# Kernel optimization log

Measured on AMD Instinct MI355X. Metric: run time of the kernel, lower is better.

Reference implementation:

```python
import jax, jax.numpy as jnp
import numpy as np

B, N, F, D, H, L, K = 128, 128, 13, 256, 8, 8, 10
FF = 2 * D  # FFN / hidden width
HEAD = D // H


def setup_inputs() -> dict:
    key = jax.random.key(0)
    ks = iter(jax.random.split(key, 64))
    def nrm(shape, scale=0.02):
        return jax.random.normal(next(ks), shape, dtype=jnp.float32) * scale
    return {
        "input_features": jax.random.normal(next(ks), (B, N, F), dtype=jnp.float32),
        "input_points": jax.random.normal(next(ks), (B, N, 2), dtype=jnp.float32),
        "input_mask": jnp.ones((B, N, 1), dtype=jnp.float32),
        "input_time": jax.random.uniform(next(ks), (B, 1), dtype=jnp.float32),
        # get_encoding: Dense(2D, gelu) -> Dense(D, gelu)
        "enc_w1": nrm((F, FF)), "enc_b1": jnp.zeros((FF,), jnp.float32),
        "enc_w2": nrm((FF, D)), "enc_b2": jnp.zeros((D,), jnp.float32),
        # FourierProjection MLP (no bias, swish)
        "four_w1": nrm((D, FF)), "four_w2": nrm((FF, D)),
        # FiLM time projection (no bias)
        "time_w": nrm((D, FF)),
        # local KNN MLPs: round 0 input 2*F, round 1 input 2*D
        "loc1_w1": nrm((2 * F, FF)), "loc1_b1": jnp.zeros((FF,), jnp.float32),
        "loc1_w2": nrm((FF, D)), "loc1_b2": jnp.zeros((D,), jnp.float32),
        "loc2_w1": nrm((2 * D, FF)), "loc2_b1": jnp.zeros((FF,), jnp.float32),
        "loc2_w2": nrm((FF, D)), "loc2_b2": jnp.zeros((D,), jnp.float32),
        # transformer encoder layers, stacked over L
        "qkv_w": nrm((L, D, 3 * D)), "qkv_b": jnp.zeros((L, 3 * D), jnp.float32),
        "out_w": nrm((L, D, D)), "out_b": jnp.zeros((L, D), jnp.float32),
        "ln1_g": jnp.ones((L, D), jnp.float32), "ln1_b": jnp.zeros((L, D), jnp.float32),
        "ff1_w": nrm((L, D, FF)), "ff1_b": jnp.zeros((L, FF), jnp.float32),
        "ff2_w": nrm((L, FF, D)), "ff2_b": jnp.zeros((L, D), jnp.float32),
        "gamma": jnp.full((L, D), 1e-5, dtype=jnp.float32),
        "ln2_g": jnp.ones((L, D), jnp.float32), "ln2_b": jnp.zeros((L, D), jnp.float32),
    }


def _ln(x, g, b, eps=1e-5):
    m = jnp.mean(x, axis=-1, keepdims=True)
    v = jnp.var(x, axis=-1, keepdims=True)
    return (x - m) * jax.lax.rsqrt(v + eps) * g + b


def _fourier(t, w1, w2):
    # t: (B,1) -> (B,D)
    half = D // 2
    emb = np.log(10000.0) / (half - 1)
    freq = jnp.exp(-emb * jnp.arange(half, dtype=jnp.float32))
    angle = t * freq[None, :] * 1000.0  # (B, half)
    e = jnp.concatenate([jnp.sin(angle), jnp.cos(angle)], axis=-1)
    e = jax.nn.silu(e @ w1)
    return jax.nn.silu(e @ w2)


def _get_neighbors(points, feats, w1, b1, w2, b2):
    # points: (B,N,P), feats: (B,N,C) -> (B,N,D)
    r = jnp.sum(points * points, axis=-1)  # (B,N)
    d = r[:, :, None] - 2.0 * jnp.einsum('bnp,bmp->bnm', points, points) + r[:, None, :]
    _, idx = jax.lax.top_k(-d, K + 1)
    idx = idx[:, :, 1:]  # drop self, (B,N,K)
    knn = jax.vmap(lambda f, i: f[i])(feats, idx)  # (B,N,K,C)
    center = jnp.broadcast_to(feats[:, :, None, :], knn.shape)
    local = jnp.concatenate([knn - center, center], axis=-1)  # (B,N,K,2C)
    local = jax.nn.gelu(local @ w1 + b1)
    local = jax.nn.gelu(local @ w2 + b2)
    return jnp.mean(local, axis=2)


def _mha(x, mask, wqkv, bqkv, wo, bo):
    Bx, Nx, _ = x.shape
    qkv = x @ wqkv + bqkv
    q, k, v = jnp.split(qkv, 3, axis=-1)
    def heads(t):
        return t.reshape(Bx, Nx, H, HEAD).transpose(0, 2, 1, 3)
    q, k, v = heads(q), heads(k), heads(v)
    scores = jnp.einsum('bhqd,bhkd->bhqk', q, k) * (1.0 / np.sqrt(HEAD))
    keep = mask[:, None, None, :, 0] > 0  # (B,1,1,N)
    scores = jnp.where(keep, scores, -1e9)
    a = jax.nn.softmax(scores, axis=-1)
    o = jnp.einsum('bhqk,bhkd->bhqd', a, v).transpose(0, 2, 1, 3).reshape(Bx, Nx, D)
    return o @ wo + bo


def _pet(input_features, input_points, input_mask, input_time,
         enc_w1, enc_b1, enc_w2, enc_b2, four_w1, four_w2, time_w,
         loc1_w1, loc1_b1, loc1_w2, loc1_b2, loc2_w1, loc2_b1, loc2_w2, loc2_b2,
         qkv_w, qkv_b, out_w, out_b, ln1_g, ln1_b, ff1_w, ff1_b, ff2_w, ff2_b,
         gamma, ln2_g, ln2_b):
    # feature encoding (RandomDrop is identity at eval / feature_drop=0)
    enc = jax.nn.gelu(input_features @ enc_w1 + enc_b1)
    enc = jax.nn.gelu(enc @ enc_w2 + enc_b2)  # (B,N,D)
    # FiLM time conditioning
    t = _fourier(input_time, four_w1, four_w2)  # (B,D)
    t = t[:, None, :] * input_mask  # (B,N,D)
    scale, shift = jnp.split(t @ time_w, 2, axis=-1)
    enc = enc * (1.0 + scale) + shift
    # local KNN aggregation
    coord_shift = 999.0 * (1.0 - input_mask)  # (B,N,1)
    points = input_points[:, :, :2]
    lf = _get_neighbors(coord_shift + points, input_features, loc1_w1, loc1_b1, loc1_w2, loc1_b2)
    lf = _get_neighbors(coord_shift + lf, lf, loc2_w1, loc2_b1, loc2_w2, loc2_b2)
    enc = enc + lf
    skip = enc
    x = enc
    for i in range(L):
        res = x
        a = _mha(x, input_mask, qkv_w[i], qkv_b[i], out_w[i], out_b[i])
        x = _ln(res + a, ln1_g[i], ln1_b[i])
        res = x
        h = jax.nn.gelu(x @ ff1_w[i] + ff1_b[i])
        h = h @ ff2_w[i] + ff2_b[i]
        h = h * gamma[i] * input_mask  # LayerScale with mask
        x = _ln(res + h, ln2_g[i], ln2_b[i])
    return x + skip


def reference(input_features, input_points, input_mask, input_time,
              enc_w1, enc_b1, enc_w2, enc_b2, four_w1, four_w2, time_w,
              loc1_w1, loc1_b1, loc1_w2, loc1_b2, loc2_w1, loc2_b1, loc2_w2, loc2_b2,
              qkv_w, qkv_b, out_w, out_b, ln1_g, ln1_b, ff1_w, ff1_b, ff2_w, ff2_b,
              gamma, ln2_g, ln2_b):
    return _pet(input_features, input_points, input_mask, input_time,
                enc_w1, enc_b1, enc_w2, enc_b2, four_w1, four_w2, time_w,
                loc1_w1, loc1_b1, loc1_w2, loc1_b2, loc2_w1, loc2_b1, loc2_w2, loc2_b2,
                qkv_w, qkv_b, out_w, out_b, ln1_g, ln1_b, ff1_w, ff1_b, ff2_w, ff2_b,
                gamma, ln2_g, ln2_b)
```

## Files before the change

kernel.cpp:

```cpp
#include <hip/hip_runtime.h>
#include <hip/hip_bf16.h>
#include <cmath>

#define DEV_INLINE __device__ __forceinline__

constexpr int Bn = 128;
constexpr int Nn = 128;
constexpr int Fn = 13;
constexpr int Dn = 256;
constexpr int Ln = 8;
constexpr int Kn = 10;
constexpr int FFn = 512;
constexpr int Tn = Bn * Nn;
constexpr int Rn = Tn * Kn;

typedef __attribute__((ext_vector_type(4))) float f32x4;
typedef __attribute__((ext_vector_type(8))) short bf16x8;
typedef unsigned short us;

__device__ float g_x[Tn * Dn];
__device__ float g_skip[Tn * Dn];
__device__ float g_big[Tn * Dn];
__device__ float g_dm[Tn * Nn];
__device__ float g_u[Bn * FFn];
__device__ float g_r[Tn];
__device__ float g_pqbias[2048];
__device__ int   g_idx[Rn];
__device__ us g_bigb[Tn * 768];
__device__ us g_xb[Tn * Dn];
__device__ us g_attb[Tn * Dn];
__device__ us g_lf1b[Tn * Dn];
__device__ us g_pq[Tn * 1024];
__device__ us g_h2b[Rn * Dn];
__device__ us g_feat16[Tn * 32];
constexpr int OFF_ENC1 = 0;
constexpr int OFF_ENC2 = OFF_ENC1 + 512 * 32;
constexpr int OFF_W2A  = OFF_ENC2 + 256 * 512;
constexpr int OFF_W2B  = OFF_W2A + 256 * 512;
constexpr int OFF_PQ1  = OFF_W2B + 256 * 512;
constexpr int OFF_PQ2  = OFF_PQ1 + 1024 * 32;
constexpr int OFF_QKV  = OFF_PQ2 + 1024 * 256;
constexpr int OFF_OUT  = OFF_QKV + 8 * 768 * 256;
constexpr int OFF_FF1  = OFF_OUT + 8 * 256 * 256;
constexpr int OFF_FF2  = OFF_FF1 + 8 * 512 * 256;
constexpr int WT_TOTAL = OFF_FF2 + 8 * 256 * 512;
__device__ us g_wt[WT_TOTAL];

DEV_INLINE float gelu_f(float x) {
    float x2 = x * x;
    float m = x * fmaf(x2, -0.07135537f, -1.59576912f);
    float t = __expf(m);
    return x * __builtin_amdgcn_rcpf(1.f + t);
}
DEV_INLINE us f2b(float x) {
    __hip_bfloat16 h = __float2bfloat16(x);
    return *(us*)&h;
}
DEV_INLINE float blo(unsigned u) { return __uint_as_float(u << 16); }
DEV_INLINE float bhi(unsigned u) { return __uint_as_float(u & 0xFFFF0000u); }
DEV_INLINE unsigned pk2(float a, float b) {
    float2 f; f.x = a; f.y = b;
    __hip_bfloat162 h = __float22bfloat162_rn(f);
    return *(unsigned*)&h;
}

#define GLOAD16(gp, lp)                                                            \
    __builtin_amdgcn_global_load_lds(                                              \
        (const __attribute__((address_space(1))) unsigned int*)(gp),               \
        (__attribute__((address_space(3))) unsigned int*)(lp), 16, 0, 0)

constexpr int UP0 = 0;
constexpr int UP1 = UP0 + 16;
constexpr int UP2 = UP1 + 128;
constexpr int UP3 = UP2 + 128;
constexpr int UP4 = UP3 + 128;
constexpr int UP5 = UP4 + 1536;
constexpr int UP6 = UP5 + 512;
constexpr int UP7 = UP6 + 1024;
constexpr int UP8 = UP7 + 1024;
constexpr int UP9 = UP8 + 1024;
constexpr int UP10 = UP9 + 1024;
constexpr int UP11 = UP10 + 2048;
constexpr int UP12 = UP11 + 128;
constexpr int UPN = UP12 + 128;

DEV_INLINE void prep_seg(const float* __restrict__ src, us* __restrict__ dst,
                         int Kreal, int Kpad, int Nd, long sstride, long dstride,
                         int gx, int gy, int lb, int tid, float* tile) {
    int z = lb / (gx * gy);
    int rem = lb - z * gx * gy;
    int by = rem / gx, bx = rem - by * gx;
    const float* s = src + (size_t)z * sstride;
    us* d = dst + (size_t)z * dstride;
    int cn = tid & 31, rk = tid >> 5;
    int kbase = by * 32, nbase = bx * 32;
#pragma unroll
    for (int p = 0; p < 4; p++) {
        int k = kbase + p * 8 + rk;
        float v = (k < Kreal) ? s[(size_t)k * Nd + nbase + cn] : 0.f;
        tile[(p * 8 + rk) * 33 + cn] = v;
    }
    __syncthreads();
#pragma unroll
    for (int p = 0; p < 4; p++) {
        int nl = p * 8 + rk;
        d[(size_t)(nbase + nl) * Kpad + kbase + cn] = f2b(tile[cn * 33 + nl]);
    }
}

DEV_INLINE void prepPQ_seg(const float* __restrict__ w1, const float* __restrict__ b1,
                           us* __restrict__ dst, float* __restrict__ bdst,
                           int Kreal, int Kpad, int n, int tid) {
    for (int k = tid; k < Kpad; k += 256) {
        float v;
        if (n < 512) v = (k < Kreal) ? w1[(size_t)k * 512 + n] : 0.f;
        else {
            int m = n - 512;
            v = (k < Kreal) ? (w1[(size_t)(Kreal + k) * 512 + m] - w1[(size_t)k * 512 + m]) : 0.f;
        }
        dst[(size_t)n * Kpad + k] = f2b(v);
    }
    if (tid == 0) bdst[n] = (n < 512) ? 0.f : b1[n - 512];
}

__global__ __launch_bounds__(256) void k_uprep(
    const float* __restrict__ enc_w1, const float* __restrict__ enc_w2,
    const float* __restrict__ l1w2, const float* __restrict__ l2w2,
    const float* __restrict__ qkv_w, const float* __restrict__ out_w,
    const float* __restrict__ ff1w, const float* __restrict__ ff2w,
    const float* __restrict__ l1w1, const float* __restrict__ l1b1,
    const float* __restrict__ l2w1, const float* __restrict__ l2b1,
    const float* __restrict__ feat, const float* __restrict__ tin,
    const float* __restrict__ four_w1, const float* __restrict__ four_w2,
    const float* __restrict__ time_w, const float* __restrict__ pts,
    const float* __restrict__ mask,
    us* __restrict__ wt, float* __restrict__ pqbias, us* __restrict__ fp,
    float* __restrict__ u, int* __restrict__ idx) {
    __shared__ float shmem[1056];
    int b = blockIdx.x, tid = threadIdx.x;
    if (b < UP1) {
        prep_seg(enc_w1, wt + OFF_ENC1, 13, 32, 512, 0, 0, 16, 1, b - UP0, tid, shmem);
    } else if (b < UP2) {
        prep_seg(enc_w2, wt + OFF_ENC2, 512, 512, 256, 0, 0, 8, 16, b - UP1, tid, shmem);
    } else if (b < UP3) {
        prep_seg(l1w2, wt + OFF_W2A, 512, 512, 256, 0, 0, 8, 16, b - UP2, tid, shmem);
    } else if (b < UP4) {
        prep_seg(l2w2, wt + OFF_W2B, 512, 512, 256, 0, 0, 8, 16, b - UP3, tid, shmem);
    } else if (b < UP5) {
        prep_seg(qkv_w, wt + OFF_QKV, 256, 256, 768, 256 * 768, 768 * 256, 24, 8, b - UP4, tid, shmem);
    } else if (b < UP6) {
        prep_seg(out_w, wt + OFF_OUT, 256, 256, 256, 256 * 256, 256 * 256, 8, 8, b - UP5, tid, shmem);
    } else if (b < UP7) {
        prep_seg(ff1w, wt + OFF_FF1, 256, 256, 512, 256 * 512, 512 * 256, 16, 8, b - UP6, tid, shmem);
    } else if (b < UP8) {
        prep_seg(ff2w, wt + OFF_FF2, 512, 512, 256, 512 * 256, 256 * 512, 8, 16, b - UP7, tid, shmem);
    } else if (b < UP9) {
        prepPQ_seg(l1w1, l1b1, wt + OFF_PQ1, pqbias, 13, 32, b - UP8, tid);
    } else if (b < UP10) {
        prepPQ_seg(l2w1, l2b1, wt + OFF_PQ2, pqbias + 1024, 256, 256, b - UP9, tid);
    } else if (b < UP11) {
        int gid = (b - UP10) * 256 + tid;
        int t = gid >> 5, c = gid & 31;
        fp[gid] = (c < Fn) ? f2b(feat[(size_t)t * Fn + c]) : (us)0;
    } else if (b < UP12) {
        float* e = shmem; float* e1 = shmem + 256; float* t2 = shmem + 768;
        int bb = b - UP11;
        float tv = tin[bb];
        if (tid < 128) {
            const float emb = 0.07252236513366287f;
            float fr = expf(-emb * (float)tid);
            float ang = tv * fr * 1000.f;
            e[tid] = sinf(ang);
            e[tid + 128] = cosf(ang);
        }
        __syncthreads();
        for (int j = tid; j < 512; j += 256) {
            float s = 0.f;
            for (int i = 0; i < 256; i++) s += e[i] * four_w1[(size_t)i * 512 + j];
            e1[j] = s / (1.f + expf(-s));
        }
        __syncthreads();
        {
            float s = 0.f;
            for (int i = 0; i < 512; i++) s += e1[i] * four_w2[(size_t)i * 256 + tid];
            t2[tid] = s / (1.f + expf(-s));
        }
        __syncthreads();
        for (int j = tid; j < 512; j += 256) {
            float s = 0.f;
            for (int i = 0; i < 256; i++) s += t2[i] * time_w[(size_t)i * 512 + j];
            u[(size_t)bb * 512 + j] = s;
        }
    } else {
        float* px = shmem; float* py = shmem + 128; float* rr = shmem + 256;
        int bb = b - UP12;
        if (tid < 128) {
            int n = tid;
            float shift = 999.f * (1.f - mask[bb * Nn + n]);
            float x = pts[(size_t)(bb * Nn + n) * 2 + 0] + shift;
            float y = pts[(size_t)(bb * Nn + n) * 2 + 1] + shift;
            px[n] = x; py[n] = y; rr[n] = x * x + y * y;
        }
        __syncthreads();
        if (tid < 128) {
            int n = tid;
            float x = px[n], y = py[n], rn = rr[n];
            float bd[Kn + 1]; int bi[Kn + 1];
#pragma unroll
            for (int j = 0; j <= Kn; j++) { bd[j] = 3.4e38f; bi[j] = -1; }
            for (int m = 0; m < Nn; m++) {
                float d = rn - 2.f * (x * px[m] + y * py[m]) + rr[m];
                if (d < bd[Kn]) {
                    int j = Kn;
                    while (j > 0 && d < bd[j - 1]) { bd[j] = bd[j - 1]; bi[j] = bi[j - 1]; j--; }
                    bd[j] = d; bi[j] = m;
                }
            }
            for (int j = 1; j <= Kn; j++) idx[(size_t)(bb * Nn + n) * Kn + j - 1] = bi[j];
        }
    }
}

template <int EPI, bool OBF>
__global__ __launch_bounds__(256) void k_mg2(const us* __restrict__ A,
                                             const us* __restrict__ Bt,
                                             const float* __restrict__ bias,
                                             void* __restrict__ Cp,
                                             int Kd, int Nd) {
    __shared__ __align__(16) us As[128 * 32];
    __shared__ __align__(16) us Bs[128 * 32];
    int tid = threadIdx.x;
    int m0 = blockIdx.y << 7, n0 = blockIdx.x << 7;
    int wave = tid >> 6, lane = tid & 63;
    int wm = (wave & 1) << 6, wn = (wave >> 1) << 6;
    int lm = lane & 15, quad = lane >> 4;
    int r0 = (wave << 5) + (lane >> 2);
    int colu = (((lane & 3) ^ ((lane >> 2) & 3)) << 3);
    const us* pa0 = A + (size_t)(m0 + r0) * Kd + colu;
    const us* pa1 = A + (size_t)(m0 + r0 + 16) * Kd + colu;
    const us* pb0 = Bt + (size_t)(n0 + r0) * Kd + colu;
    const us* pb1 = Bt + (size_t)(n0 + r0 + 16) * Kd + colu;
    auto lAs = (__attribute__((address_space(3))) us*)As;
    auto lBs = (__attribute__((address_space(3))) us*)Bs;
    int lbase = wave << 10;
    int fcol = ((quad ^ (lm & 3)) << 3);
    f32x4 acc[4][4] = {};
    for (int k0 = 0; k0 < Kd; k0 += 32) {
        __syncthreads();
        GLOAD16(pa0 + k0, lAs + lbase);
        GLOAD16(pa1 + k0, lAs + lbase + 512);
        GLOAD16(pb0 + k0, lBs + lbase);
        GLOAD16(pb1 + k0, lBs + lbase + 512);
        __syncthreads();
        bf16x8 afr[4], bfr[4];
#pragma unroll
        for (int i = 0; i < 4; i++) {
            afr[i] = *(const bf16x8*)&As[(wm + i * 16 + lm) * 32 + fcol];
            bfr[i] = *(const bf16x8*)&Bs[(wn + i * 16 + lm) * 32 + fcol];
        }
#pragma unroll
        for (int mf = 0; mf < 4; mf++)
#pragma unroll
            for (int nf = 0; nf < 4; nf++)
                acc[mf][nf] = __builtin_amdgcn_mfma_f32_16x16x32_bf16(afr[mf], bfr[nf], acc[mf][nf], 0, 0, 0);
    }
    float bvs[4];
#pragma unroll
    for (int nf = 0; nf < 4; nf++) bvs[nf] = bias[n0 + wn + nf * 16 + lm];
#pragma unroll
    for (int mf = 0; mf < 4; mf++) {
#pragma unroll
        for (int r = 0; r < 4; r++) {
            size_t row = (size_t)(m0 + wm + mf * 16 + (quad << 2) + r);
#pragma unroll
            for (int nf = 0; nf < 4; nf++) {
                float v = acc[mf][nf][r] + bvs[nf];
                if (EPI == 1) v = gelu_f(v);
                size_t ci = row * Nd + n0 + wn + nf * 16 + lm;
                if constexpr (OBF) ((us*)Cp)[ci] = f2b(v);
                else ((float*)Cp)[ci] = v;
            }
        }
    }
}

template <bool PM, bool FINAL>
__global__ __launch_bounds__(512) void k_mgln(const us* __restrict__ A,
                                              const us* __restrict__ Bt,
                                              const float* __restrict__ bias,
                                              const us* __restrict__ res,
                                              const float* __restrict__ gamma,
                                              const float* __restrict__ mask,
                                              const float* __restrict__ lng,
                                              const float* __restrict__ lnb,
                                              const float* __restrict__ skip,
                                              us* __restrict__ xbout,
                                              float* __restrict__ finout,
                                              int Kd) {
    __shared__ __align__(16) us As[128 * 32];
    __shared__ __align__(16) us Bs[256 * 32];
    __shared__ float2 part[4][128];
    __shared__ float2 stat[128];
    int tid = threadIdx.x;
    int m0 = blockIdx.x << 7;
    int wave = tid >> 6, lane = tid & 63;
    int wm = (wave & 1) << 6, wn = (wave >> 1) << 6;
    int grp = wave >> 1;
    int lm = lane & 15, quad = lane >> 4;
    int ar = (wave << 4) + (lane >> 2);
    int br = (wave << 5) + (lane >> 2);
    int colu = (((lane & 3) ^ ((lane >> 2) & 3)) << 3);
    const us* pa = A + (size_t)(m0 + ar) * Kd + colu;
    const us* pb0 = Bt + (size_t)br * Kd + colu;
    const us* pb1 = Bt + (size_t)(br + 16) * Kd + colu;
    auto lAs = (__attribute__((address_space(3))) us*)As;
    auto lBs = (__attribute__((address_space(3))) us*)Bs;
    int fcol = ((quad ^ (lm & 3)) << 3);
    f32x4 acc[4][4] = {};
    for (int k0 = 0; k0 < Kd; k0 += 32) {
        __syncthreads();
        GLOAD16(pa + k0, lAs + (wave << 9));
        GLOAD16(pb0 + k0, lBs + (wave << 10));
        GLOAD16(pb1 + k0, lBs + (wave << 10) + 512);
        __syncthreads();
        bf16x8 afr[4], bfr[4];
#pragma unroll
        for (int i = 0; i < 4; i++) {
            afr[i] = *(const bf16x8*)&As[(wm + i * 16 + lm) * 32 + fcol];
            bfr[i] = *(const bf16x8*)&Bs[(wn + i * 16 + lm) * 32 + fcol];
        }
#pragma unroll
        for (int mf = 0; mf < 4; mf++)
#pragma unroll
            for (int nf = 0; nf < 4; nf++)
                acc[mf][nf] = __builtin_amdgcn_mfma_f32_16x16x32_bf16(afr[mf], bfr[nf], acc[mf][nf], 0, 0, 0);
    }
    float bvs[4], gms[4];
#pragma unroll
    for (int nf = 0; nf < 4; nf++) {
        int col = wn + nf * 16 + lm;
        bvs[nf] = bias[col];
        if (PM) gms[nf] = gamma[col];
    }
#pragma unroll
    for (int mf = 0; mf < 4; mf++) {
#pragma unroll
        for (int r = 0; r < 4; r++) {
            int rowl = wm + mf * 16 + (quad << 2) + r;
            size_t row = (size_t)(m0 + rowl);
            float mrow = PM ? mask[row] : 0.f;
            float s1 = 0.f, s2 = 0.f;
#pragma unroll
            for (int nf = 0; nf < 4; nf++) {
                int col = wn + nf * 16 + lm;
                float rv = blo((unsigned)res[row * 256 + col]);
                float v = acc[mf][nf][r] + bvs[nf];
                v = PM ? fmaf(v * gms[nf], mrow, rv) : rv + v;
                acc[mf][nf][r] = v;
                s1 += v; s2 += v * v;
            }
            s1 += __shfl_xor(s1, 1, 64); s2 += __shfl_xor(s2, 1, 64);
            s1 += __shfl_xor(s1, 2, 64); s2 += __shfl_xor(s2, 2, 64);
            s1 += __shfl_xor(s1, 4, 64); s2 += __shfl_xor(s2, 4, 64);
            s1 += __shfl_xor(s1, 8, 64); s2 += __shfl_xor(s2, 8, 64);
            if (lm == 0) { float2 p; p.x = s1; p.y = s2; part[grp][rowl] = p; }
        }
    }
    __syncthreads();
    if (tid < 128) {
        float2 p0 = part[0][tid], p1 = part[1][tid], p2 = part[2][tid], p3 = part[3][tid];
        float s = p0.x + p1.x + p2.x + p3.x;
        float q = p0.y + p1.y + p2.y + p3.y;
        float mean = s * (1.f / 256.f);
        float var = q * (1.f / 256.f) - mean * mean;
        float2 st; st.x = mean; st.y = rsqrtf(var + 1e-5f);
        stat[tid] = st;
    }
    __syncthreads();
    float gvs[4], bts[4];
#pragma unroll
    for (int nf = 0; nf < 4; nf++) {
        int col = wn + nf * 16 + lm;
        gvs[nf] = lng[col];
        bts[nf] = lnb[col];
    }
#pragma unroll
    for (int mf = 0; mf < 4; mf++) {
#pragma unroll
        for (int r = 0; r < 4; r++) {
            int rowl = wm + mf * 16 + (quad << 2) + r;
            size_t row = (size_t)(m0 + rowl);
            float2 st = stat[rowl];
#pragma unroll
            for (int nf = 0; nf < 4; nf++) {
                int col = wn + nf * 16 + lm;
                float nv = fmaf((acc[mf][nf][r] - st.x) * st.y, gvs[nf], bts[nf]);
                if (FINAL) finout[row * 256 + col] = nv + skip[row * 256 + col];
                else xbout[row * 256 + col] = f2b(nv);
            }
        }
    }
}

__global__ __launch_bounds__(512) void k_knng(const us* __restrict__ pq,
                                              const int* __restrict__ idx,
                                              const us* __restrict__ Bt,
                                              const float* __restrict__ bias,
                                              us* __restrict__ h2b) {
    __shared__ __align__(16) us As[128 * 64];
    __shared__ __align__(16) us Bs[256 * 64];
    int tid = threadIdx.x;
    int m0 = blockIdx.x << 7;
    int wave = tid >> 6, lane = tid & 63;
    int wm = (wave & 1) << 6, wn = (wave >> 1) << 6;
    int lm = lane & 15, quad = lane >> 4;
    int arow = tid >> 2, acolu = (tid & 3) << 4;
    int asw = arow & 7;
    int ablk0 = ((tid & 3) << 1) ^ asw, ablk1 = (((tid & 3) << 1) + 1) ^ asw;
    int r = m0 + arow;
    int tok = r / 10;
    int nb = idx[r];
    int prow = (tok & ~127) + nb;
    const us* Pp = pq + (size_t)prow * 1024 + acolu;
    const us* Qp = pq + (size_t)tok * 1024 + 512 + acolu;
    int brow = (wave << 5) + (lane >> 3);
    int bcol = (((lane & 7) ^ (lane >> 3)) << 3);
    const us* pb = Bt + (size_t)brow * 512 + bcol;
    auto lBs = (__attribute__((address_space(3))) us*)Bs;
    int lbase = wave << 11;
    int fsw = lm & 7;
    f32x4 acc[4][4] = {};
    for (int k0 = 0; k0 < 512; k0 += 64) {
        uint4 pv0 = *(const uint4*)(Pp + k0);
        uint4 pv1 = *(const uint4*)(Pp + k0 + 8);
        uint4 qv0 = *(const uint4*)(Qp + k0);
        uint4 qv1 = *(const uint4*)(Qp + k0 + 8);
        uint4 h0, h1;
        h0.x = pk2(gelu_f(blo(pv0.x) + blo(qv0.x)), gelu_f(bhi(pv0.x) + bhi(qv0.x)));
        h0.y = pk2(gelu_f(blo(pv0.y) + blo(qv0.y)), gelu_f(bhi(pv0.y) + bhi(qv0.y)));
        h0.z = pk2(gelu_f(blo(pv0.z) + blo(qv0.z)), gelu_f(bhi(pv0.z) + bhi(qv0.z)));
        h0.w = pk2(gelu_f(blo(pv0.w) + blo(qv0.w)), gelu_f(bhi(pv0.w) + bhi(qv0.w)));
        h1.x = pk2(gelu_f(blo(pv1.x) + blo(qv1.x)), gelu_f(bhi(pv1.x) + bhi(qv1.x)));
        h1.y = pk2(gelu_f(blo(pv1.y) + blo(qv1.y)), gelu_f(bhi(pv1.y) + bhi(qv1.y)));
        h1.z = pk2(gelu_f(blo(pv1.z) + blo(qv1.z)), gelu_f(bhi(pv1.z) + bhi(qv1.z)));
        h1.w = pk2(gelu_f(blo(pv1.w) + blo(qv1.w)), gelu_f(bhi(pv1.w) + bhi(qv1.w)));
        __syncthreads();
        GLOAD16(pb + k0, lBs + lbase);
        GLOAD16(pb + k0 + 8 * 512, lBs + lbase + 512);
        GLOAD16(pb + k0 + 16 * 512, lBs + lbase + 1024);
        GLOAD16(pb + k0 + 24 * 512, lBs + lbase + 1536);
        *(uint4*)&As[arow * 64 + (ablk0 << 3)] = h0;
        *(uint4*)&As[arow * 64 + (ablk1 << 3)] = h1;
        __syncthreads();
#pragma unroll
        for (int sub = 0; sub < 2; sub++) {
            int lblk = (sub << 2) + quad;
            int fcol = ((lblk ^ fsw) << 3);
            bf16x8 afr[4], bfr[4];
#pragma unroll
            for (int i = 0; i < 4; i++) {
                afr[i] = *(const bf16x8*)&As[(wm + i * 16 + lm) * 64 + fcol];
                bfr[i] = *(const bf16x8*)&Bs[(wn + i * 16 + lm) * 64 + fcol];
            }
#pragma unroll
            for (int mf = 0; mf < 4; mf++)
#pragma unroll
                for (int nf = 0; nf < 4; nf++)
                    acc[mf][nf] = __builtin_amdgcn_mfma_f32_16x16x32_bf16(afr[mf], bfr[nf], acc[mf][nf], 0, 0, 0);
        }
    }
    float bvs[4];
#pragma unroll
    for (int nf = 0; nf < 4; nf++) bvs[nf] = bias[wn + nf * 16 + lm];
#pragma unroll
    for (int mf = 0; mf < 4; mf++) {
#pragma unroll
        for (int rr = 0; rr < 4; rr++) {
            size_t row = (size_t)(m0 + wm + mf * 16 + (quad << 2) + rr);
#pragma unroll
            for (int nf = 0; nf < 4; nf++) {
                float v = gelu_f(acc[mf][nf][rr] + bvs[nf]);
                h2b[row * 256 + wn + nf * 16 + lm] = f2b(v);
            }
        }
    }
}

__global__ __launch_bounds__(64) void k_mean1s(const us* __restrict__ h2b,
                                               const float* __restrict__ mask,
                                               us* __restrict__ lfb,
                                               float* __restrict__ big,
                                               float* __restrict__ r) {
    int t = blockIdx.x, lane = threadIdx.x;
    int c = lane << 2;
    const us* p = h2b + (size_t)t * Kn * 256 + c;
    float s0 = 0.f, s1 = 0.f, s2 = 0.f, s3 = 0.f;
#pragma unroll
    for (int k = 0; k < Kn; k++) {
        uint2 v = *(const uint2*)(p + k * 256);
        s0 += blo(v.x); s1 += bhi(v.x);
        s2 += blo(v.y); s3 += bhi(v.y);
    }
    s0 *= 0.1f; s1 *= 0.1f; s2 *= 0.1f; s3 *= 0.1f;
    uint2 ob; ob.x = pk2(s0, s1); ob.y = pk2(s2, s3);
    *(uint2*)&lfb[(size_t)t * 256 + c] = ob;
    float sh = 999.f * (1.f - mask[t]);
    float4 w; w.x = s0 + sh; w.y = s1 + sh; w.z = s2 + sh; w.w = s3 + sh;
    *(float4*)&big[(size_t)t * 256 + c] = w;
    float sq = w.x * w.x + w.y * w.y + w.z * w.z + w.w * w.w;
#pragma unroll
    for (int off = 32; off; off >>= 1) sq += __shfl_xor(sq, off, 64);
    if (lane == 0) r[t] = sq;
}

__global__ __launch_bounds__(256) void k_dist(const float* __restrict__ fe,
                                              const float* __restrict__ r,
                                              float* __restrict__ Dm) {
    int b = blockIdx.z;
    int m0 = blockIdx.x * 64, n0 = blockIdx.y * 64;
    const float* A = fe + (size_t)b * Nn * Dn;
    __shared__ float As[16][68];
    __shared__ float Bs[16][68];
    int tid = threadIdx.x;
    int tx = tid & 15, ty = tid >> 4;
    int ar = tid >> 2, ac = (tid & 3) << 2;
    float acc[4][4] = {};
    for (int k0 = 0; k0 < Dn; k0 += 16) {
        float4 av = *(const float4*)&A[(size_t)(n0 + ar) * Dn + k0 + ac];
        float4 bv = *(const float4*)&A[(size_t)(m0 + ar) * Dn + k0 + ac];
        __syncthreads();
        As[ac + 0][ar] = av.x; As[ac + 1][ar] = av.y; As[ac + 2][ar] = av.z; As[ac + 3][ar] = av.w;
        Bs[ac + 0][ar] = bv.x; Bs[ac + 1][ar] = bv.y; Bs[ac + 2][ar] = bv.z; Bs[ac + 3][ar] = bv.w;
        __syncthreads();
#pragma unroll
        for (int kk = 0; kk < 16; kk++) {
            float4 a = *(const float4*)&As[kk][ty << 2];
            float4 b2 = *(const float4*)&Bs[kk][tx << 2];
            acc[0][0] += a.x * b2.x; acc[0][1] += a.x * b2.y; acc[0][2] += a.x * b2.z; acc[0][3] += a.x * b2.w;
            acc[1][0] += a.y * b2.x; acc[1][1] += a.y * b2.y; acc[1][2] += a.y * b2.z; acc[1][3] += a.y * b2.w;
            acc[2][0] += a.z * b2.x; acc[2][1] += a.z * b2.y; acc[2][2] += a.z * b2.z; acc[2][3] += a.z * b2.w;
            acc[3][0] += a.w * b2.x; acc[3][1] += a.w * b2.y; acc[3][2] += a.w * b2.z; acc[3][3] += a.w * b2.w;
        }
    }
    float4 rm = *(const float4*)&r[b * Nn + m0 + (tx << 2)];
#pragma unroll
    for (int i = 0; i < 4; i++) {
        int n = n0 + (ty << 2) + i;
        float rn = r[b * Nn + n];
        float4 v;
        v.x = rn - 2.f * acc[i][0] + rm.x;
        v.y = rn - 2.f * acc[i][1] + rm.y;
        v.z = rn - 2.f * acc[i][2] + rm.z;
        v.w = rn - 2.f * acc[i][3] + rm.w;
        *(float4*)&Dm[(size_t)b * Nn * Nn + (size_t)n * Nn + m0 + (tx << 2)] = v;
    }
}

__global__ __launch_bounds__(128) void k_topkg(const float* __restrict__ Dm, int* __restrict__ idx) {
    int b = blockIdx.x, n = threadIdx.x;
    const float* row = Dm + (size_t)b * Nn * Nn + (size_t)n * Nn;
    float bd[Kn + 1]; int bi[Kn + 1];
#pragma unroll
    for (int j = 0; j <= Kn; j++) { bd[j] = 3.4e38f; bi[j] = -1; }
    for (int m = 0; m < Nn; m++) {
        float d = row[m];
        if (d < bd[Kn]) {
            int j = Kn;
            while (j > 0 && d < bd[j - 1]) { bd[j] = bd[j - 1]; bi[j] = bi[j - 1]; j--; }
            bd[j] = d; bi[j] = m;
        }
    }
    for (int j = 1; j <= Kn; j++) idx[(size_t)(b * Nn + n) * Kn + j - 1] = bi[j];
}

__global__ __launch_bounds__(256) void k_meanc(const us* __restrict__ h2b,
                                               const float* __restrict__ u,
                                               const float* __restrict__ mask,
                                               const float* __restrict__ x,
                                               float* __restrict__ skip,
                                               us* __restrict__ xb) {
    int t = blockIdx.x, c = threadIdx.x;
    const us* p = h2b + (size_t)t * Kn * 256 + c;
    float s = 0.f;
#pragma unroll
    for (int k = 0; k < Kn; k++) s += blo((unsigned)p[k * 256]);
    s *= 0.1f;
    int b = t >> 7;
    float m = mask[t];
    float xv = x[(size_t)t * Dn + c];
    float sc = u[(size_t)b * 512 + c];
    float sh = u[(size_t)b * 512 + 256 + c];
    float v = xv * (1.f + m * sc) + m * sh + s;
    skip[(size_t)t * Dn + c] = v;
    xb[(size_t)t * Dn + c] = f2b(v);
}

__global__ __launch_bounds__(256) void k_attn(const us* __restrict__ qkv,
                                              const float* __restrict__ mask,
                                              us* __restrict__ outp) {
    __shared__ __align__(16) us Qs[128 * 40];
    __shared__ __align__(16) us Ks[128 * 40];
    __shared__ __align__(16) us Vt[32 * 136];
    __shared__ __align__(16) us Ps[128 * 136];
    __shared__ float msk[128];
    int bh = blockIdx.x;
    int b = bh >> 3, h = bh & 7;
    int tid = threadIdx.x;
    int wave = tid >> 6, lane = tid & 63;
    int lm = lane & 15, quad = lane >> 4;
    int wm = wave << 5;
    {
        int row = tid >> 1, off = (tid & 1) << 4;
        const us* rp = qkv + (size_t)(b * 128 + row) * 768 + h * 32 + off;
        *(uint4*)&Qs[row * 40 + off] = *(const uint4*)(rp);
        *(uint4*)&Qs[row * 40 + off + 8] = *(const uint4*)(rp + 8);
        *(uint4*)&Ks[row * 40 + off] = *(const uint4*)(rp + 256);
        *(uint4*)&Ks[row * 40 + off + 8] = *(const uint4*)(rp + 264);
        union { uint4 u[2]; us s[16]; } tv;
        tv.u[0] = *(const uint4*)(rp + 512);
        tv.u[1] = *(const uint4*)(rp + 520);
#pragma unroll
        for (int j = 0; j < 16; j++) Vt[(off + j) * 136 + row] = tv.s[j];
        if (tid < 128) msk[tid] = mask[b * 128 + tid];
    }
    __syncthreads();
    f32x4 acc[2][8] = {};
    {
        bf16x8 aq[2];
#pragma unroll
        for (int mf = 0; mf < 2; mf++)
            aq[mf] = *(const bf16x8*)&Qs[(wm + mf * 16 + lm) * 40 + (quad << 3)];
#pragma unroll
        for (int nf = 0; nf < 8; nf++) {
            bf16x8 bk = *(const bf16x8*)&Ks[(nf * 16 + lm) * 40 + (quad << 3)];
            acc[0][nf] = __builtin_amdgcn_mfma_f32_16x16x32_bf16(aq[0], bk, acc[0][nf], 0, 0, 0);
            acc[1][nf] = __builtin_amdgcn_mfma_f32_16x16x32_bf16(aq[1], bk, acc[1][nf], 0, 0, 0);
        }
    }
    {
        const float sc = 0.17677669529663687f;
        float mkc[8];
#pragma unroll
        for (int nf = 0; nf < 8; nf++) mkc[nf] = msk[nf * 16 + lm];
#pragma unroll
        for (int mf = 0; mf < 2; mf++) {
#pragma unroll
            for (int nf = 0; nf < 8; nf++)
#pragma unroll
                for (int r = 0; r < 4; r++) {
                    float s = acc[mf][nf][r];
                    acc[mf][nf][r] = mkc[nf] > 0.f ? s * sc : -1.0e9f;
                }
#pragma unroll
            for (int r = 0; r < 4; r++) {
                float m = acc[mf][0][r];
#pragma unroll
                for (int nf = 1; nf < 8; nf++) m = fmaxf(m, acc[mf][nf][r]);
                m = fmaxf(m, __shfl_xor(m, 1, 64));
                m = fmaxf(m, __shfl_xor(m, 2, 64));
                m = fmaxf(m, __shfl_xor(m, 4, 64));
                m = fmaxf(m, __shfl_xor(m, 8, 64));
                float s = 0.f;
#pragma unroll
                for (int nf = 0; nf < 8; nf++) {
                    float p = __expf(acc[mf][nf][r] - m);
                    acc[mf][nf][r] = p;
                    s += p;
                }
                s += __shfl_xor(s, 1, 64);
                s += __shfl_xor(s, 2, 64);
                s += __shfl_xor(s, 4, 64);
                s += __shfl_xor(s, 8, 64);
                float linv = __builtin_amdgcn_rcpf(s);
                int prow = wm + mf * 16 + (quad << 2) + r;
#pragma unroll
                for (int nf = 0; nf < 8; nf++)
                    Ps[prow * 136 + nf * 16 + lm] = f2b(acc[mf][nf][r] * linv);
            }
        }
    }
    __syncthreads();
    f32x4 oacc[2][2] = {};
    for (int kt = 0; kt < 4; kt++) {
        bf16x8 ap[2], bv[2];
#pragma unroll
        for (int mf = 0; mf < 2; mf++)
            ap[mf] = *(const bf16x8*)&Ps[(wm + mf * 16 + lm) * 136 + kt * 32 + (quad << 3)];
#pragma unroll
        for (int nf = 0; nf < 2; nf++)
            bv[nf] = *(const bf16x8*)&Vt[(nf * 16 + lm) * 136 + kt * 32 + (quad << 3)];
#pragma unroll
        for (int mf = 0; mf < 2; mf++)
#pragma unroll
            for (int nf = 0; nf < 2; nf++)
                oacc[mf][nf] = __builtin_amdgcn_mfma_f32_16x16x32_bf16(ap[mf], bv[nf], oacc[mf][nf], 0, 0, 0);
    }
#pragma unroll
    for (int mf = 0; mf < 2; mf++)
#pragma unroll
        for (int r = 0; r < 4; r++) {
            int row = wm + mf * 16 + (quad << 2) + r;
#pragma unroll
            for (int nf = 0; nf < 2; nf++)
                outp[(size_t)(b * 128 + row) * 256 + h * 32 + nf * 16 + lm] = f2b(oacc[mf][nf][r]);
        }
}

extern "C" void kernel_launch(void* const* d_in, const int* in_sizes, int n_in,
                              void* d_out, int out_size, void* d_ws, size_t ws_size,
                              hipStream_t stream) {
    (void)in_sizes; (void)n_in; (void)out_size; (void)d_ws; (void)ws_size;
    const float* f_feat = (const float*)d_in[0];
    const float* f_pts  = (const float*)d_in[1];
    const float* f_mask = (const float*)d_in[2];
    const float* f_time = (const float*)d_in[3];
    const float* enc_w1 = (const float*)d_in[4];
    const float* enc_b1 = (const float*)d_in[5];
    const float* enc_w2 = (const float*)d_in[6];
    const float* enc_b2 = (const float*)d_in[7];
    const float* four_w1 = (const float*)d_in[8];
    const float* four_w2 = (const float*)d_in[9];
    const float* time_w = (const float*)d_in[10];
    const float* l1w1 = (const float*)d_in[11];
    const float* l1b1 = (const float*)d_in[12];
    const float* l1w2 = (const float*)d_in[13];
    const float* l1b2 = (const float*)d_in[14];
    const float* l2w1 = (const float*)d_in[15];
    const float* l2b1 = (const float*)d_in[16];
    const float* l2w2 = (const float*)d_in[17];
    const float* l2b2 = (const float*)d_in[18];
    const float* qkv_w = (const float*)d_in[19];
    const float* qkv_b = (const float*)d_in[20];
    const float* out_w = (const float*)d_in[21];
    const float* out_b = (const float*)d_in[22];
    const float* ln1g = (const float*)d_in[23];
    const float* ln1b = (const float*)d_in[24];
    const float* ff1w = (const float*)d_in[25];
    const float* ff1b = (const float*)d_in[26];
    const float* ff2w = (const float*)d_in[27];
    const float* ff2b = (const float*)d_in[28];
    const float* gam  = (const float*)d_in[29];
    const float* ln2g = (const float*)d_in[30];
    const float* ln2b = (const float*)d_in[31];
    float* out = (float*)d_out;

    float *x, *skip, *big, *dm, *u, *r, *pqbias;
    int* idx;
    us *bigb, *xb, *attb, *lf1b, *pq, *h2b, *feat16, *wt;
    hipGetSymbolAddress((void**)&x,    HIP_SYMBOL(g_x));
    hipGetSymbolAddress((void**)&skip, HIP_SYMBOL(g_skip));
    hipGetSymbolAddress((void**)&big,  HIP_SYMBOL(g_big));
    hipGetSymbolAddress((void**)&dm,   HIP_SYMBOL(g_dm));
    hipGetSymbolAddress((void**)&u,    HIP_SYMBOL(g_u));
    hipGetSymbolAddress((void**)&r,    HIP_SYMBOL(g_r));
    hipGetSymbolAddress((void**)&pqbias, HIP_SYMBOL(g_pqbias));
    hipGetSymbolAddress((void**)&idx,  HIP_SYMBOL(g_idx));
    hipGetSymbolAddress((void**)&bigb, HIP_SYMBOL(g_bigb));
    hipGetSymbolAddress((void**)&xb,   HIP_SYMBOL(g_xb));
    hipGetSymbolAddress((void**)&attb, HIP_SYMBOL(g_attb));
    hipGetSymbolAddress((void**)&lf1b, HIP_SYMBOL(g_lf1b));
    hipGetSymbolAddress((void**)&pq,   HIP_SYMBOL(g_pq));
    hipGetSymbolAddress((void**)&h2b,  HIP_SYMBOL(g_h2b));
    hipGetSymbolAddress((void**)&feat16, HIP_SYMBOL(g_feat16));
    hipGetSymbolAddress((void**)&wt,   HIP_SYMBOL(g_wt));

    k_uprep<<<UPN, 256, 0, stream>>>(
        enc_w1, enc_w2, l1w2, l2w2, qkv_w, out_w, ff1w, ff2w,
        l1w1, l1b1, l2w1, l2b1, f_feat, f_time, four_w1, four_w2, time_w,
        f_pts, f_mask, wt, pqbias, feat16, u, idx);

    k_mg2<1, true><<<dim3(4, 128), 256, 0, stream>>>(feat16, wt + OFF_ENC1, enc_b1, bigb, 32, 512);
    k_mg2<1, false><<<dim3(2, 128), 256, 0, stream>>>(bigb, wt + OFF_ENC2, enc_b2, x, 512, 256);
    k_mg2<0, true><<<dim3(8, 128), 256, 0, stream>>>(feat16, wt + OFF_PQ1, pqbias, pq, 32, 1024);
    k_knng<<<Rn / 128, 512, 0, stream>>>(pq, idx, wt + OFF_W2A, l1b2, h2b);
    k_mean1s<<<Tn, 64, 0, stream>>>(h2b, f_mask, lf1b, big, r);
    k_dist<<<dim3(2, 2, Bn), 256, 0, stream>>>(big, r, dm);
    k_topkg<<<Bn, Nn, 0, stream>>>(dm, idx);
    k_mg2<0, true><<<dim3(8, 128), 256, 0, stream>>>(lf1b, wt + OFF_PQ2, pqbias + 1024, pq, 256, 1024);
    k_knng<<<Rn / 128, 512, 0, stream>>>(pq, idx, wt + OFF_W2B, l2b2, h2b);
    k_meanc<<<Tn, 256, 0, stream>>>(h2b, u, f_mask, x, skip, xb);
    for (int l = 0; l < Ln; l++) {
        k_mg2<0, true><<<dim3(6, 128), 256, 0, stream>>>(
            xb, wt + OFF_QKV + (size_t)l * 768 * 256, qkv_b + l * 768, bigb, 256, 768);
        k_attn<<<Bn * 8, 256, 0, stream>>>(bigb, f_mask, attb);
        k_mgln<false, false><<<128, 512, 0, stream>>>(
            attb, wt + OFF_OUT + (size_t)l * 256 * 256, out_b + l * 256,
            xb, nullptr, f_mask, ln1g + l * Dn, ln1b + l * Dn, nullptr, xb, nullptr, 256);
        k_mg2<1, true><<<dim3(4, 128), 256, 0, stream>>>(
            xb, wt + OFF_FF1 + (size_t)l * 512 * 256, ff1b + l * 512, bigb, 256, 512);
        if (l < Ln - 1)
            k_mgln<true, false><<<128, 512, 0, stream>>>(
                bigb, wt + OFF_FF2 + (size_t)l * 256 * 512, ff2b + l * 256,
                xb, gam + l * Dn, f_mask, ln2g + l * Dn, ln2b + l * Dn, nullptr, xb, nullptr, 512);
        else
            k_mgln<true, true><<<128, 512, 0, stream>>>(
                bigb, wt + OFF_FF2 + (size_t)l * 256 * 512, ff2b + l * 256,
                xb, gam + l * Dn, f_mask, ln2g + l * Dn, ln2b + l * Dn, skip, nullptr, out, 512);
    }
}
```

Baseline: 1.511 ms.

## Fuse transformer layer loop into one persistent cooperative kernel with grid syncs

Replaces the per-layer chain of QKV GEMM, attention, out-projection+LN, FF1 and FF2+LN launches with one cooperative kernel of 256 blocks. Each block walks tiles of every stage, with grid-wide syncs between stages. Attention is reworked so each block handles four (batch, head) units, with every wave covering 16 query rows. The aim is to remove about 40 kernel launches and their gaps. In exchange there are 40 grid barriers, a fixed grid that leaves half the blocks idle in the LN stages and runs the QKV stage unevenly, and less parallelism in attention than the former 1024-block launch.

```diff
diff --git a/kernel.cpp b/kernel.cpp
--- a/kernel.cpp
+++ b/kernel.cpp
@@ -1,6 +1,9 @@
 #include <hip/hip_runtime.h>
+#include <hip/hip_cooperative_groups.h>
 #include <hip/hip_bf16.h>
 #include <cmath>
+
+namespace cg = cooperative_groups;
 
 #define DEV_INLINE __device__ __forceinline__
 
@@ -284,25 +287,72 @@
     }
 }
 
+template <int EPI>
+DEV_INLINE void dev_gemm(const us* __restrict__ A, const us* __restrict__ Bt,
+                         const float* __restrict__ bias, us* __restrict__ C,
+                         int Kd, int Ndc, int m0, int n0, char* smem, int tid) {
+    us* As = (us*)smem;
+    us* Bs = (us*)(smem + 8192);
+    int wave = tid >> 6, lane = tid & 63;
+    int wm = (wave & 1) << 6, wn = (wave >> 1) << 6;
+    int lm = lane & 15, quad = lane >> 4;
+    int ar = (wave << 4) + (lane >> 2);
+    int br = (wave << 5) + (lane >> 2);
+    int colu = (((lane & 3) ^ ((lane >> 2) & 3)) << 3);
+    const us* pa = A + (size_t)(m0 + ar) * Kd + colu;
+    const us* pb0 = Bt + (size_t)(n0 + br) * Kd + colu;
+    const us* pb1 = Bt + (size_t)(n0 + br + 16) * Kd + colu;
+    auto lAs = (__attribute__((address_space(3))) us*)As;
+    auto lBs = (__attribute__((address_space(3))) us*)Bs;
+    int fcol = ((quad ^ (lm & 3)) << 3);
+    f32x4 acc[4][4] = {};
+    for (int k0 = 0; k0 < Kd; k0 += 32) {
+        __syncthreads();
+        GLOAD16(pa + k0, lAs + (wave << 9));
+        GLOAD16(pb0 + k0, lBs + (wave << 10));
+        GLOAD16(pb1 + k0, lBs + (wave << 10) + 512);
+        __syncthreads();
+        bf16x8 afr[4], bfr[4];
+#pragma unroll
+        for (int i = 0; i < 4; i++) {
+            afr[i] = *(const bf16x8*)&As[(wm + i * 16 + lm) * 32 + fcol];
+            bfr[i] = *(const bf16x8*)&Bs[(wn + i * 16 + lm) * 32 + fcol];
+        }
+#pragma unroll
+        for (int mf = 0; mf < 4; mf++)
+#pragma unroll
+            for (int nf = 0; nf < 4; nf++)
+                acc[mf][nf] = __builtin_amdgcn_mfma_f32_16x16x32_bf16(afr[mf], bfr[nf], acc[mf][nf], 0, 0, 0);
+    }
+    float bvs[4];
+#pragma unroll
+    for (int nf = 0; nf < 4; nf++) bvs[nf] = bias[n0 + wn + nf * 16 + lm];
+#pragma unroll
+    for (int mf = 0; mf < 4; mf++) {
+#pragma unroll
+        for (int r = 0; r < 4; r++) {
+            size_t row = (size_t)(m0 + wm + mf * 16 + (quad << 2) + r);
+#pragma unroll
+            for (int nf = 0; nf < 4; nf++) {
+                float v = acc[mf][nf][r] + bvs[nf];
+                if (EPI == 1) v = gelu_f(v);
+                C[row * Ndc + n0 + wn + nf * 16 + lm] = f2b(v);
+            }
+        }
+    }
+}
+
 template <bool PM, bool FINAL>
-__global__ __launch_bounds__(512) void k_mgln(const us* __restrict__ A,
-                                              const us* __restrict__ Bt,
-                                              const float* __restrict__ bias,
-                                              const us* __restrict__ res,
-                                              const float* __restrict__ gamma,
-                                              const float* __restrict__ mask,
-                                              const float* __restrict__ lng,
-                                              const float* __restrict__ lnb,
-                                              const float* __restrict__ skip,
-                                              us* __restrict__ xbout,
-                                              float* __restrict__ finout,
-                                              int Kd) {
-    __shared__ __align__(16) us As[128 * 32];
-    __shared__ __align__(16) us Bs[256 * 32];
-    __shared__ float2 part[4][128];
-    __shared__ float2 stat[128];
-    int tid = threadIdx.x;
-    int m0 = blockIdx.x << 7;
+DEV_INLINE void dev_mgln(const us* __restrict__ A, const us* __restrict__ Bt,
+                         const float* __restrict__ bias, const us* __restrict__ res,
+                         const float* __restrict__ gamma, const float* __restrict__ mask,
+                         const float* __restrict__ lng, const float* __restrict__ lnb,
+                         const float* __restrict__ skip, us* __restrict__ xbout,
+                         float* __restrict__ finout, int Kd, int m0, char* smem, int tid) {
+    us* As = (us*)smem;
+    us* Bs = (us*)(smem + 8192);
+    float2* part = (float2*)(smem + 24576);
+    float2* stat = (float2*)(smem + 28672);
     int wave = tid >> 6, lane = tid & 63;
     int wm = (wave & 1) << 6, wn = (wave >> 1) << 6;
     int grp = wave >> 1;
@@ -363,12 +413,12 @@
             s1 += __shfl_xor(s1, 2, 64); s2 += __shfl_xor(s2, 2, 64);
             s1 += __shfl_xor(s1, 4, 64); s2 += __shfl_xor(s2, 4, 64);
             s1 += __shfl_xor(s1, 8, 64); s2 += __shfl_xor(s2, 8, 64);
-            if (lm == 0) { float2 p; p.x = s1; p.y = s2; part[grp][rowl] = p; }
+            if (lm == 0) { float2 p; p.x = s1; p.y = s2; part[grp * 128 + rowl] = p; }
         }
     }
     __syncthreads();
     if (tid < 128) {
-        float2 p0 = part[0][tid], p1 = part[1][tid], p2 = part[2][tid], p3 = part[3][tid];
+        float2 p0 = part[tid], p1 = part[128 + tid], p2 = part[256 + tid], p3 = part[384 + tid];
         float s = p0.x + p1.x + p2.x + p3.x;
         float q = p0.y + p1.y + p2.y + p3.y;
         float mean = s * (1.f / 256.f);
@@ -399,6 +449,151 @@
                 else xbout[row * 256 + col] = f2b(nv);
             }
         }
+    }
+    __syncthreads();
+}
+
+DEV_INLINE void dev_attn(int u, const us* __restrict__ qkv, const float* __restrict__ mask,
+                         us* __restrict__ attb, char* smem, int tid) {
+    us* Qs = (us*)smem;
+    us* Ks = (us*)(smem + 10240);
+    us* Vt = (us*)(smem + 20480);
+    us* Ps = (us*)(smem + 29184);
+    float* msk = (float*)(smem + 64000);
+    int b = u >> 3, h = u & 7;
+    int wave = tid >> 6, lane = tid & 63;
+    int lm = lane & 15, quad = lane >> 4;
+    int wm = wave << 4;
+    {
+        int row = tid >> 2, off = (tid & 3) << 3;
+        const us* rp = qkv + (size_t)(b * 128 + row) * 768 + h * 32 + off;
+        *(uint4*)&Qs[row * 40 + off] = *(const uint4*)(rp);
+        *(uint4*)&Ks[row * 40 + off] = *(const uint4*)(rp + 256);
+        union { uint4 uu; us s[8]; } tv;
+        tv.uu = *(const uint4*)(rp + 512);
+#pragma unroll
+        for (int j = 0; j < 8; j++) Vt[(off + j) * 136 + row] = tv.s[j];
+        if (tid < 128) msk[tid] = mask[b * 128 + tid];
+    }
+    __syncthreads();
+    f32x4 acc[8] = {};
+    bf16x8 aq = *(const bf16x8*)&Qs[(wm + lm) * 40 + (quad << 3)];
+#pragma unroll
+    for (int nf = 0; nf < 8; nf++) {
+        bf16x8 bk = *(const bf16x8*)&Ks[(nf * 16 + lm) * 40 + (quad << 3)];
+        acc[nf] = __builtin_amdgcn_mfma_f32_16x16x32_bf16(aq, bk, acc[nf], 0, 0, 0);
+    }
+    const float sc = 0.17677669529663687f;
+    float mkc[8];
+#pragma unroll
+    for (int nf = 0; nf < 8; nf++) mkc[nf] = msk[nf * 16 + lm];
+#pragma unroll
+    for (int nf = 0; nf < 8; nf++)
+#pragma unroll
+        for (int r = 0; r < 4; r++)
+            acc[nf][r] = mkc[nf] > 0.f ? acc[nf][r] * sc : -1.0e9f;
+#pragma unroll
+    for (int r = 0; r < 4; r++) {
+        float m = acc[0][r];
+#pragma unroll
+        for (int nf = 1; nf < 8; nf++) m = fmaxf(m, acc[nf][r]);
+        m = fmaxf(m, __shfl_xor(m, 1, 64));
+        m = fmaxf(m, __shfl_xor(m, 2, 64));
+        m = fmaxf(m, __shfl_xor(m, 4, 64));
+        m = fmaxf(m, __shfl_xor(m, 8, 64));
+        float s = 0.f;
+#pragma unroll
+        for (int nf = 0; nf < 8; nf++) {
+            float p = __expf(acc[nf][r] - m);
+            acc[nf][r] = p;
+            s += p;
+        }
+        s += __shfl_xor(s, 1, 64);
+        s += __shfl_xor(s, 2, 64);
+        s += __shfl_xor(s, 4, 64);
+        s += __shfl_xor(s, 8, 64);
+        float linv = __builtin_amdgcn_rcpf(s);
+        int prow = wm + (quad << 2) + r;
+#pragma unroll
+        for (int nf = 0; nf < 8; nf++)
+            Ps[prow * 136 + nf * 16 + lm] = f2b(acc[nf][r] * linv);
+    }
+    __syncthreads();
+    f32x4 oacc[2] = {};
+#pragma unroll
+    for (int kt = 0; kt < 4; kt++) {
+        bf16x8 ap = *(const bf16x8*)&Ps[(wm + lm) * 136 + kt * 32 + (quad << 3)];
+#pragma unroll
+        for (int nf = 0; nf < 2; nf++) {
+            bf16x8 bv = *(const bf16x8*)&Vt[(nf * 16 + lm) * 136 + kt * 32 + (quad << 3)];
+            oacc[nf] = __builtin_amdgcn_mfma_f32_16x16x32_bf16(ap, bv, oacc[nf], 0, 0, 0);
+        }
+    }
+#pragma unroll
+    for (int r = 0; r < 4; r++) {
+        int row = wm + (quad << 2) + r;
+#pragma unroll
+        for (int nf = 0; nf < 2; nf++)
+            attb[(size_t)(b * 128 + row) * 256 + h * 32 + nf * 16 + lm] = f2b(oacc[nf][r]);
+    }
+    __syncthreads();
+}
+
+__global__ __launch_bounds__(512) void k_layers(
+    const us* __restrict__ wt, const float* __restrict__ qkv_b,
+    const float* __restrict__ out_b, const float* __restrict__ ff1b,
+    const float* __restrict__ ff2b, const float* __restrict__ ln1g,
+    const float* __restrict__ ln1b, const float* __restrict__ ln2g,
+    const float* __restrict__ ln2b, const float* __restrict__ gam,
+    const float* __restrict__ mask, const float* __restrict__ skip,
+    us* __restrict__ xb, us* __restrict__ bigb, us* __restrict__ attb,
+    float* __restrict__ outp) {
+    __shared__ __align__(16) char smem[64512];
+    cg::grid_group grid = cg::this_grid();
+    int tid = threadIdx.x;
+    int bid = blockIdx.x;
+    for (int l = 0; l < Ln; l++) {
+        {
+            const us* Bt = wt + OFF_QKV + (size_t)l * 768 * 256;
+            const float* bias = qkv_b + l * 768;
+            for (int t = bid; t < 384; t += 256)
+                dev_gemm<0>(xb, Bt, bias, bigb, 256, 768, (t / 3) << 7, (t % 3) << 8, smem, tid);
+        }
+        grid.sync();
+        for (int u = bid * 4; u < bid * 4 + 4; u++)
+            dev_attn(u, bigb, mask, attb, smem, tid);
+        grid.sync();
+        {
+            const us* Bt = wt + OFF_OUT + (size_t)l * 256 * 256;
+            for (int t = bid; t < 128; t += 256)
+                dev_mgln<false, false>(attb, Bt, out_b + l * 256, xb, nullptr, mask,
+                                       ln1g + l * Dn, ln1b + l * Dn, nullptr, xb, nullptr,
+                                       256, t << 7, smem, tid);
+        }
+        grid.sync();
+        {
+            const us* Bt = wt + OFF_FF1 + (size_t)l * 512 * 256;
+            const float* bias = ff1b + l * 512;
+            for (int t = bid; t < 256; t += 256)
+                dev_gemm<1>(xb, Bt, bias, bigb, 256, 512, (t >> 1) << 7, (t & 1) << 8, smem, tid);
+        }
+        grid.sync();
+        {
+            const us* Bt = wt + OFF_FF2 + (size_t)l * 256 * 512;
+            const float* bias = ff2b + l * 256;
+            if (l < Ln - 1) {
+                for (int t = bid; t < 128; t += 256)
+                    dev_mgln<true, false>(bigb, Bt, bias, xb, gam + l * Dn, mask,
+                                          ln2g + l * Dn, ln2b + l * Dn, nullptr, xb, nullptr,
+                                          512, t << 7, smem, tid);
+            } else {
+                for (int t = bid; t < 128; t += 256)
+                    dev_mgln<true, true>(bigb, Bt, bias, xb, gam + l * Dn, mask,
+                                         ln2g + l * Dn, ln2b + l * Dn, skip, nullptr, outp,
+                                         512, t << 7, smem, tid);
+            }
+        }
+        grid.sync();
     }
 }
 
@@ -595,117 +790,6 @@
     xb[(size_t)t * Dn + c] = f2b(v);
 }
 
-__global__ __launch_bounds__(256) void k_attn(const us* __restrict__ qkv,
-                                              const float* __restrict__ mask,
-                                              us* __restrict__ outp) {
-    __shared__ __align__(16) us Qs[128 * 40];
-    __shared__ __align__(16) us Ks[128 * 40];
-    __shared__ __align__(16) us Vt[32 * 136];
-    __shared__ __align__(16) us Ps[128 * 136];
-    __shared__ float msk[128];
-    int bh = blockIdx.x;
-    int b = bh >> 3, h = bh & 7;
-    int tid = threadIdx.x;
-    int wave = tid >> 6, lane = tid & 63;
-    int lm = lane & 15, quad = lane >> 4;
-    int wm = wave << 5;
-    {
-        int row = tid >> 1, off = (tid & 1) << 4;
-        const us* rp = qkv + (size_t)(b * 128 + row) * 768 + h * 32 + off;
-        *(uint4*)&Qs[row * 40 + off] = *(const uint4*)(rp);
-        *(uint4*)&Qs[row * 40 + off + 8] = *(const uint4*)(rp + 8);
-        *(uint4*)&Ks[row * 40 + off] = *(const uint4*)(rp + 256);
-        *(uint4*)&Ks[row * 40 + off + 8] = *(const uint4*)(rp + 264);
-        union { uint4 u[2]; us s[16]; } tv;
-        tv.u[0] = *(const uint4*)(rp + 512);
-        tv.u[1] = *(const uint4*)(rp + 520);
-#pragma unroll
-        for (int j = 0; j < 16; j++) Vt[(off + j) * 136 + row] = tv.s[j];
-        if (tid < 128) msk[tid] = mask[b * 128 + tid];
-    }
-    __syncthreads();
-    f32x4 acc[2][8] = {};
-    {
-        bf16x8 aq[2];
-#pragma unroll
-        for (int mf = 0; mf < 2; mf++)
-            aq[mf] = *(const bf16x8*)&Qs[(wm + mf * 16 + lm) * 40 + (quad << 3)];
-#pragma unroll
-        for (int nf = 0; nf < 8; nf++) {
-            bf16x8 bk = *(const bf16x8*)&Ks[(nf * 16 + lm) * 40 + (quad << 3)];
-            acc[0][nf] = __builtin_amdgcn_mfma_f32_16x16x32_bf16(aq[0], bk, acc[0][nf], 0, 0, 0);
-            acc[1][nf] = __builtin_amdgcn_mfma_f32_16x16x32_bf16(aq[1], bk, acc[1][nf], 0, 0, 0);
-        }
-    }
-    {
-        const float sc = 0.17677669529663687f;
-        float mkc[8];
-#pragma unroll
-        for (int nf = 0; nf < 8; nf++) mkc[nf] = msk[nf * 16 + lm];
-#pragma unroll
-        for (int mf = 0; mf < 2; mf++) {
-#pragma unroll
-            for (int nf = 0; nf < 8; nf++)
-#pragma unroll
-                for (int r = 0; r < 4; r++) {
-                    float s = acc[mf][nf][r];
-                    acc[mf][nf][r] = mkc[nf] > 0.f ? s * sc : -1.0e9f;
-                }
-#pragma unroll
-            for (int r = 0; r < 4; r++) {
-                float m = acc[mf][0][r];
-#pragma unroll
-                for (int nf = 1; nf < 8; nf++) m = fmaxf(m, acc[mf][nf][r]);
-                m = fmaxf(m, __shfl_xor(m, 1, 64));
-                m = fmaxf(m, __shfl_xor(m, 2, 64));
-                m = fmaxf(m, __shfl_xor(m, 4, 64));
-                m = fmaxf(m, __shfl_xor(m, 8, 64));
-                float s = 0.f;
-#pragma unroll
-                for (int nf = 0; nf < 8; nf++) {
-                    float p = __expf(acc[mf][nf][r] - m);
-                    acc[mf][nf][r] = p;
-                    s += p;
-                }
-                s += __shfl_xor(s, 1, 64);
-                s += __shfl_xor(s, 2, 64);
-                s += __shfl_xor(s, 4, 64);
-                s += __shfl_xor(s, 8, 64);
-                float linv = __builtin_amdgcn_rcpf(s);
-                int prow = wm + mf * 16 + (quad << 2) + r;
-#pragma unroll
-                for (int nf = 0; nf < 8; nf++)
-                    Ps[prow * 136 + nf * 16 + lm] = f2b(acc[mf][nf][r] * linv);
-            }
-        }
-    }
-    __syncthreads();
-    f32x4 oacc[2][2] = {};
-    for (int kt = 0; kt < 4; kt++) {
-        bf16x8 ap[2], bv[2];
-#pragma unroll
-        for (int mf = 0; mf < 2; mf++)
-            ap[mf] = *(const bf16x8*)&Ps[(wm + mf * 16 + lm) * 136 + kt * 32 + (quad << 3)];
-#pragma unroll
-        for (int nf = 0; nf < 2; nf++)
-            bv[nf] = *(const bf16x8*)&Vt[(nf * 16 + lm) * 136 + kt * 32 + (quad << 3)];
-#pragma unroll
-        for (int mf = 0; mf < 2; mf++)
-#pragma unroll
-            for (int nf = 0; nf < 2; nf++)
-                oacc[mf][nf] = __builtin_amdgcn_mfma_f32_16x16x32_bf16(ap[mf], bv[nf], oacc[mf][nf], 0, 0, 0);
-    }
-#pragma unroll
-    for (int mf = 0; mf < 2; mf++)
-#pragma unroll
-        for (int r = 0; r < 4; r++) {
-            int row = wm + mf * 16 + (quad << 2) + r;
-#pragma unroll
-            for (int nf = 0; nf < 2; nf++)
-                outp[(size_t)(b * 128 + row) * 256 + h * 32 + nf * 16 + lm] = f2b(oacc[mf][nf][r]);
-        }
-}
-
 extern "C" void kernel_launch(void* const* d_in, const int* in_sizes, int n_in,
                               void* d_out, int out_size, void* d_ws, size_t ws_size,
                               hipStream_t stream) {
@@ -779,22 +863,11 @@
     k_mg2<0, true><<<dim3(8, 128), 256, 0, stream>>>(lf1b, wt + OFF_PQ2, pqbias + 1024, pq, 256, 1024);
     k_knng<<<Rn / 128, 512, 0, stream>>>(pq, idx, wt + OFF_W2B, l2b2, h2b);
     k_meanc<<<Tn, 256, 0, stream>>>(h2b, u, f_mask, x, skip, xb);
-    for (int l = 0; l < Ln; l++) {
-        k_mg2<0, true><<<dim3(6, 128), 256, 0, stream>>>(
-            xb, wt + OFF_QKV + (size_t)l * 768 * 256, qkv_b + l * 768, bigb, 256, 768);
-        k_attn<<<Bn * 8, 256, 0, stream>>>(bigb, f_mask, attb);
-        k_mgln<false, false><<<128, 512, 0, stream>>>(
-            attb, wt + OFF_OUT + (size_t)l * 256 * 256, out_b + l * 256,
-            xb, nullptr, f_mask, ln1g + l * Dn, ln1b + l * Dn, nullptr, xb, nullptr, 256);
-        k_mg2<1, true><<<dim3(4, 128), 256, 0, stream>>>(
-            xb, wt + OFF_FF1 + (size_t)l * 512 * 256, ff1b + l * 512, bigb, 256, 512);
-        if (l < Ln - 1)
-            k_mgln<true, false><<<128, 512, 0, stream>>>(
-                bigb, wt + OFF_FF2 + (size_t)l * 256 * 512, ff2b + l * 256,
-                xb, gam + l * Dn, f_mask, ln2g + l * Dn, ln2b + l * Dn, nullptr, xb, nullptr, 512);
-        else
-            k_mgln<true, true><<<128, 512, 0, stream>>>(
-                bigb, wt + OFF_FF2 + (size_t)l * 256 * 512, ff2b + l * 256,
-                xb, gam + l * Dn, f_mask, ln2g + l * Dn, ln2b + l * Dn, skip, nullptr, out, 512);
-    }
-}
+
+    void* kargs[] = {
+        (void*)&wt, (void*)&qkv_b, (void*)&out_b, (void*)&ff1b, (void*)&ff2b,
+        (void*)&ln1g, (void*)&ln1b, (void*)&ln2g, (void*)&ln2b, (void*)&gam,
+        (void*)&f_mask, (void*)&skip, (void*)&xb, (void*)&bigb, (void*)&attb,
+        (void*)&out};
+    hipLaunchCooperativeKernel((void*)k_layers, dim3(256), dim3(512), kargs, 0, stream);
+}
```

Result: slower. 2.900 ms (+91.9%).
